# Performance work log

Measured on AMD Instinct MI355X. Metric: run time of the kernel, lower is better.

The kernel has to match this reference:

```python
import jax, jax.numpy as jnp
import numpy as np

G = 4          # conv groups (hardcoded in module)
C = 1024       # channels (hardcoded cin=cout=1024)
SCALE = 1.0 / np.sqrt(1024.0).astype(np.float32)  # 1/sqrt(c/h), h=1


def grouped_proj(x, W, b):
    # pointwise grouped Conv1d == block-diagonal matmul over channel groups
    # x: [B, C, P], W: [G, C//G out, C//G in], b: [C]
    B, C_, P = x.shape
    xg = x.reshape(B, G, C_ // G, P)
    y = jnp.einsum('goi,bgip->bgop', W, xg)  # [B, G, C//G, P]
    return y.reshape(B, C_, P) + b[None, :, None]


def setup_inputs() -> dict:
    key = jax.random.key(0)
    ks = jax.random.split(key, 8)
    B, PK, PQ = 8, 1024, 4096
    cg = C // G
    w_std = 1.0 / np.sqrt(cg).astype(np.float32)  # ~ conv default init scale
    return {
        'Xq': jax.random.normal(ks[0], (B, C, PQ), jnp.float32),
        'Xk': jax.random.normal(ks[1], (B, C, PK), jnp.float32),
        'Wq': jax.random.normal(ks[2], (G, cg, cg), jnp.float32) * w_std,
        'bq': jax.random.normal(ks[3], (C,), jnp.float32) * 0.01,
        'Wk': jax.random.normal(ks[4], (G, cg, cg), jnp.float32) * w_std,
        'bk': jax.random.normal(ks[5], (C,), jnp.float32) * 0.01,
        'Wv': jax.random.normal(ks[6], (G, cg, cg), jnp.float32) * w_std,
        'bv': jax.random.normal(ks[7], (C,), jnp.float32) * 0.01,
    }


def reference(Xq, Xk, Wq, bq, Wk, bk, Wv, bv):
    # Q and K are both projected from Xk; V from Xq (as in the torch code)
    Q = grouped_proj(Xk, Wq, bq)   # [B, C, Pk]
    K = grouped_proj(Xk, Wk, bk)   # [B, C, Pk]
    V = grouped_proj(Xq, Wv, bv)   # [B, C, Pq]
    b, c, pk = K.shape
    pq = V.shape[-1]
    h = 1
    Qh = Q.reshape(b, h, c // h, pk)
    Kh = K.reshape(b, h, c // h, pk)
    Vh = V.reshape(b, h, c // h, pq)
    # H: [B, h, Pk, Pq], contraction over channels; softmax over dim=-2 (Pk)
    H = jnp.einsum('bhci,bhcj->bhij', Kh, Vh) * SCALE
    H = jax.nn.softmax(H, axis=-2)
    # sparse_constrain: Gram over last axis vs identity, mean squared error
    mid = jnp.einsum('bhci,bhki->bhck', H, H)          # [B, h, Pk, Pk]
    Iden = jnp.eye(pk, dtype=H.dtype)[None, None]       # broadcast over B, h
    sparse_loss = jnp.mean((mid - Iden) ** 2)
    # out: mix Q along Pk with attention H -> [B, h, C, Pq]
    out = jnp.einsum('bhij,bhki->bhkj', H, Qh).reshape(b, c, pq)
    return out, sparse_loss, H
```

## Files before the change

### kernel.cpp

```cpp
#include <hip/hip_runtime.h>

typedef _Float16 f16;
typedef f16 f16x4 __attribute__((ext_vector_type(4)));
typedef f16 f16x8 __attribute__((ext_vector_type(8)));
typedef float f32x4 __attribute__((ext_vector_type(4)));

__device__ __forceinline__ void gload16(const void* g, void* ldsbase) {
  __builtin_amdgcn_global_load_lds((const __attribute__((address_space(1))) unsigned int*)g,
                                   (__attribute__((address_space(3))) unsigned int*)ldsbase, 16, 0, 0);
}

__device__ __forceinline__ int swz(int row, int c) {
  return row * 64 + ((c ^ ((row >> 1) & 3)) << 4);
}

template<int MODE>
__global__ void __launch_bounds__(512, 2)
gemm256(const f16* __restrict__ A, const f16* __restrict__ Bm, float* __restrict__ Cf,
        f16* __restrict__ E16, f16* __restrict__ E16t,
        int K, long sA, long sB, float scale, float* __restrict__ aux) {
  __shared__ f16 sb[65536];
  const int t = threadIdx.x, l = t & 63, w = t >> 6;
  const int wr = w >> 2, wc = w & 3;
  const int bid = blockIdx.x;
  const int swzb = (bid & 7) * 64 + (bid >> 3);
  const long b = swzb >> 6;
  const int inner = swzb & 63;
  const int bx = inner >> 2, by = inner & 3;
  const char* Abyte = (const char*)(A + b * sA + (long)(by * 256) * K);
  const char* Bbyte = (const char*)(Bm + b * sB + (long)(bx * 256) * K);

  int offSrc[4];
#pragma unroll
  for (int i = 0; i < 4; ++i) {
    int cid = i * 512 + t, row = cid >> 3, slot = cid & 7;
    offSrc[i] = row * (K * 2) + ((slot ^ (row & 7)) << 4);
  }
  int offAf[8][2], offBf[4][2];
#pragma unroll
  for (int mi = 0; mi < 8; ++mi) {
    int r = wr * 128 + mi * 16 + (l & 15);
#pragma unroll
    for (int ks = 0; ks < 2; ++ks)
      offAf[mi][ks] = r * 64 + ((((ks << 2) + (l >> 4)) ^ (r & 7)) << 3);
  }
#pragma unroll
  for (int ni = 0; ni < 4; ++ni) {
    int r = wc * 64 + ni * 16 + (l & 15);
#pragma unroll
    for (int ks = 0; ks < 2; ++ks)
      offBf[ni][ks] = r * 64 + ((((ks << 2) + (l >> 4)) ^ (r & 7)) << 3);
  }

  const int NT = K >> 6;
  f32x4 acc[8][4] = {};

  auto STAGE = [&](int kt, int bsel) {
    f16* la = sb + bsel * 32768;
    f16* lb = la + 16384;
    const char* as = Abyte + (long)kt * 128;
    const char* bs = Bbyte + (long)kt * 128;
#pragma unroll
    for (int i = 0; i < 4; ++i)
      gload16(as + offSrc[i], la + (i * 512 + (w << 6)) * 8);
#pragma unroll
    for (int i = 0; i < 4; ++i)
      gload16(bs + offSrc[i], lb + (i * 512 + (w << 6)) * 8);
  };

  STAGE(0, 0);
  for (int kt = 0; kt < NT; ++kt) {
    const int cur = kt & 1;
    if (kt + 1 < NT) {
      STAGE(kt + 1, cur ^ 1);
      asm volatile("s_waitcnt vmcnt(8)" ::: "memory");
    } else {
      asm volatile("s_waitcnt vmcnt(0)" ::: "memory");
    }
    __builtin_amdgcn_s_barrier();
    asm volatile("" ::: "memory");
    const f16* la = sb + cur * 32768;
    const f16* lb = la + 16384;
#pragma unroll
    for (int ks = 0; ks < 2; ++ks) {
      f16x8 bf[4];
#pragma unroll
      for (int ni = 0; ni < 4; ++ni) bf[ni] = *(const f16x8*)(lb + offBf[ni][ks]);
#pragma unroll
      for (int mi = 0; mi < 8; ++mi) {
        f16x8 af = *(const f16x8*)(la + offAf[mi][ks]);
#pragma unroll
        for (int ni = 0; ni < 4; ++ni)
          acc[mi][ni] = __builtin_amdgcn_mfma_f32_16x16x32_f16(af, bf[ni], acc[mi][ni], 0, 0, 0);
      }
    }
    asm volatile("s_waitcnt lgkmcnt(0)" ::: "memory");
    __builtin_amdgcn_s_barrier();
    asm volatile("" ::: "memory");
  }

  const int i0 = by * 256, j0 = bx * 256;
  if (MODE == 2) {
    float csum[4] = {};
#pragma unroll
    for (int mi = 0; mi < 8; ++mi)
#pragma unroll
      for (int ni = 0; ni < 4; ++ni)
#pragma unroll
        for (int q = 0; q < 4; ++q) {
          float e = __expf(acc[mi][ni][q] * scale);
          acc[mi][ni][q] = e;
          csum[ni] += e;
        }
#pragma unroll
    for (int ni = 0; ni < 4; ++ni) {
      csum[ni] += __shfl_xor(csum[ni], 16);
      csum[ni] += __shfl_xor(csum[ni], 32);
    }
    float* colp = (float*)(sb + 34816);
    if (l < 16) {
#pragma unroll
      for (int ni = 0; ni < 4; ++ni) colp[wr * 256 + wc * 64 + ni * 16 + l] = csum[ni];
    }
    __syncthreads();
    if (t < 256) aux[(b * 4 + by) * 4096 + bx * 256 + t] = colp[t] + colp[256 + t];
    f16* E16b = E16 + b * 4194304L;
    f16* E16tb = E16t + b * 4194304L;
#pragma unroll
    for (int s = 0; s < 4; ++s) {
      if (wr == (s >> 1)) {
        const int h = s & 1;
#pragma unroll
        for (int m2 = 0; m2 < 4; ++m2)
#pragma unroll
          for (int ni = 0; ni < 4; ++ni)
#pragma unroll
            for (int q = 0; q < 4; ++q)
              sb[(m2 * 16 + (l >> 4) * 4 + q) * 264 + wc * 64 + ni * 16 + (l & 15)] =
                  (f16)acc[h * 4 + m2][ni][q];
      }
      __syncthreads();
#pragma unroll
      for (int ii = 0; ii < 4; ++ii) {
        int cid = ii * 512 + t, r = cid >> 5, cc = cid & 31;
        *(f16x8*)(E16b + (long)(i0 + s * 64 + r) * 4096 + j0 + cc * 8) =
            *(const f16x8*)(sb + r * 264 + cc * 8);
      }
      const int q4 = w >> 1, r8 = l >> 3, ic = l & 7;
#pragma unroll
      for (int ii = 0; ii < 4; ++ii) {
        int j = q4 * 64 + r8 * 8 + (w & 1) * 4 + ii;
        f16x8 v;
#pragma unroll
        for (int k2 = 0; k2 < 8; ++k2) v[k2] = sb[(ic * 8 + k2) * 264 + j];
        *(f16x8*)(E16tb + (long)(j0 + j) * 1024 + i0 + s * 64 + ic * 8) = v;
      }
      __syncthreads();
    }
  } else {
    const float* ip = aux + b * 4096 + bx * 256 + wc * 64;
    float iv[4];
#pragma unroll
    for (int ni = 0; ni < 4; ++ni) iv[ni] = ip[ni * 16 + (l & 15)];
    float* Cb = Cf + b * 4194304L + (long)(by * 256 + wr * 128) * 4096 + bx * 256 + wc * 64;
#pragma unroll
    for (int mi = 0; mi < 8; ++mi)
#pragma unroll
      for (int ni = 0; ni < 4; ++ni)
#pragma unroll
        for (int q = 0; q < 4; ++q)
          Cb[(long)(mi * 16 + (l >> 4) * 4 + q) * 4096 + ni * 16 + (l & 15)] = acc[mi][ni][q] * iv[ni];
  }
}

__global__ void __launch_bounds__(512, 2)
gram_p(const f16* __restrict__ E, const f16* __restrict__ inv2sg,
       float* __restrict__ Hf, float* __restrict__ parts) {
  __shared__ f16 sb[69632];
  const int t = threadIdx.x, l = t & 63, w = t >> 6;
  const int wr = w >> 2, wc = w & 3;
  const int bid = blockIdx.x;
  const long b = bid & 7;
  const int inner = bid >> 3;
  const int by = inner >> 2, bx = inner & 3;
  const char* Abyte = (const char*)(E + b * 4194304L + (long)(by * 256) * 4096);
  const char* Bbyte = (const char*)(E + b * 4194304L + (long)(bx * 256) * 4096);
  f16* invl = sb + 65536;
  gload16((const char*)(inv2sg + b * 4096) + (long)t * 16, invl + (w << 6) * 8);
  int offSrc[4];
#pragma unroll
  for (int i = 0; i < 4; ++i) {
    int cid = i * 512 + t, row = cid >> 3, slot = cid & 7;
    offSrc[i] = row * 8192 + ((slot ^ (row & 7)) << 4);
  }
  int offAf[8][2], offBf[4][2];
#pragma unroll
  for (int mi = 0; mi < 8; ++mi) {
    int r = wr * 128 + mi * 16 + (l & 15);
#pragma unroll
    for (int ks = 0; ks < 2; ++ks)
      offAf[mi][ks] = r * 64 + ((((ks << 2) + (l >> 4)) ^ (r & 7)) << 3);
  }
#pragma unroll
  for (int ni = 0; ni < 4; ++ni) {
    int r = wc * 64 + ni * 16 + (l & 15);
#pragma unroll
    for (int ks = 0; ks < 2; ++ks)
      offBf[ni][ks] = r * 64 + ((((ks << 2) + (l >> 4)) ^ (r & 7)) << 3);
  }
  f32x4 acc[8][4] = {};
  auto STAGE = [&](int kt, int bsel) {
    f16* la = sb + bsel * 32768;
    f16* lb = la + 16384;
    const char* as = Abyte + (long)kt * 128;
    const char* bs = Bbyte + (long)kt * 128;
#pragma unroll
    for (int i = 0; i < 4; ++i) gload16(as + offSrc[i], la + (i * 512 + (w << 6)) * 8);
#pragma unroll
    for (int i = 0; i < 4; ++i) gload16(bs + offSrc[i], lb + (i * 512 + (w << 6)) * 8);
  };
  const int kw0 = bx * 16;
  STAGE(0, 0);
  for (int kt = 0; kt < 64; ++kt) {
    const int cur = kt & 1;
    if (kt + 1 < 64) {
      STAGE(kt + 1, cur ^ 1);
      if (kt - 1 >= kw0 && kt - 1 < kw0 + 16) asm volatile("s_waitcnt vmcnt(40)" ::: "memory");
      else                                    asm volatile("s_waitcnt vmcnt(8)" ::: "memory");
    } else {
      asm volatile("s_waitcnt vmcnt(0)" ::: "memory");
    }
    __builtin_amdgcn_s_barrier();
    asm volatile("" ::: "memory");
    const f16* la = sb + cur * 32768;
    const f16* lb = la + 16384;
#pragma unroll
    for (int ks = 0; ks < 2; ++ks) {
      const f16x8 invv = *(const f16x8*)(invl + kt * 64 + ks * 32 + ((l >> 4) << 3));
      f16x8 bf[4];
#pragma unroll
      for (int ni = 0; ni < 4; ++ni) bf[ni] = *(const f16x8*)(lb + offBf[ni][ks]);
#pragma unroll
      for (int mi = 0; mi < 8; ++mi) {
        f16x8 af = *(const f16x8*)(la + offAf[mi][ks]) * invv;
#pragma unroll
        for (int ni = 0; ni < 4; ++ni)
          acc[mi][ni] = __builtin_amdgcn_mfma_f32_16x16x32_f16(af, bf[ni], acc[mi][ni], 0, 0, 0);
      }
    }
    if (kt >= kw0 && kt < kw0 + 16) {
      const float iv = sqrtf((float)invl[kt * 64 + l]) * (1.0f / 64.0f);
      float* hp = Hf + b * 4194304L + (long)(by * 256 + w * 32) * 4096 + kt * 64 + l;
#pragma unroll
      for (int rr = 0; rr < 32; ++rr) {
        const int row = w * 32 + rr;
        f16 ev = la[row * 64 + ((((l >> 3) ^ (row & 7)) << 3) | (l & 7))];
        hp[(long)rr * 4096] = (float)ev * iv;
      }
    }
    asm volatile("s_waitcnt lgkmcnt(0)" ::: "memory");
    __builtin_amdgcn_s_barrier();
    asm volatile("" ::: "memory");
  }
  const int gr0 = by * 256 + wr * 128 + (l >> 4) * 4;
  const int gc0 = bx * 256 + wc * 64 + (l & 15);
  float p = 0.f;
#pragma unroll
  for (int mi = 0; mi < 8; ++mi)
#pragma unroll
    for (int ni = 0; ni < 4; ++ni)
#pragma unroll
      for (int q = 0; q < 4; ++q) {
        float e = acc[mi][ni][q] * (1.0f / 4096.0f);
        if (gr0 + mi * 16 + q == gc0 + ni * 16) e -= 1.f;
        p += e * e;
      }
#pragma unroll
  for (int d = 32; d; d >>= 1) p += __shfl_down(p, d);
  __shared__ float red[8];
  if (l == 0) red[w] = p;
  __syncthreads();
  if (t == 0) {
    float s = 0.f;
#pragma unroll
    for (int i = 0; i < 8; ++i) s += red[i];
    parts[bid] = s;
  }
}

__global__ void __launch_bounds__(512)
proj_qk(const float* __restrict__ X, const f16* __restrict__ Wq16, const f16* __restrict__ Wk16,
        const float* __restrict__ bq, const float* __restrict__ bk,
        f16* __restrict__ Q, f16* __restrict__ Kt) {
  __shared__ f16 sb[20480];
  f16* Wqs = sb;
  f16* Wks = sb + 8192;
  f16* Xs = sb + 16384;
  const int t = threadIdx.x, l = t & 63, w = t >> 6;
  const int wrq = w >> 1, wcq = w & 1;
  const int bg = blockIdx.z, g = bg & 3;
  const long b = bg >> 2;
  const int p0 = blockIdx.x * 128;
  const float* Xb = X + b * 1048576 + (long)g * 262144;
  const char* WqB = (const char*)(Wq16 + g * 65536);
  const char* WkB = (const char*)(Wk16 + g * 65536);
  int wOff[2];
#pragma unroll
  for (int i = 0; i < 2; ++i) {
    int c = i * 512 + t, row = c >> 2, slot = (c & 3) ^ ((row >> 1) & 3);
    wOff[i] = row * 512 + (slot << 4);
  }
  const int xp = t & 127, xc = t >> 7;
  const float* xS = Xb + (long)(xc * 8) * 1024 + p0 + xp;
  const int xo = swz(xp, xc);
  int offW[4], offX[4];
#pragma unroll
  for (int i = 0; i < 4; ++i) {
    int rc = wrq * 64 + i * 16 + (l & 15);
    offW[i] = swz(rc, l >> 4);
    int rp = wcq * 64 + i * 16 + (l & 15);
    offX[i] = swz(rp, l >> 4);
  }
  f32x4 accq[4][4] = {}, acck[4][4] = {};
  for (int k0 = 0; k0 < 256; k0 += 32) {
#pragma unroll
    for (int i = 0; i < 2; ++i) {
      gload16(WqB + wOff[i] + k0 * 2, Wqs + (i * 512 + (w << 6)) * 8);
      gload16(WkB + wOff[i] + k0 * 2, Wks + (i * 512 + (w << 6)) * 8);
    }
    const float* xs = xS + (long)k0 * 1024;
    f16x8 v;
#pragma unroll
    for (int d = 0; d < 8; ++d) v[d] = (f16)xs[(long)d * 1024];
    *(f16x8*)((char*)Xs + xo) = v;
    __syncthreads();
    f16x8 qf[4], kf[4], xf[4];
#pragma unroll
    for (int i = 0; i < 4; ++i) {
      qf[i] = *(const f16x8*)((const char*)Wqs + offW[i]);
      kf[i] = *(const f16x8*)((const char*)Wks + offW[i]);
      xf[i] = *(const f16x8*)((const char*)Xs + offX[i]);
    }
#pragma unroll
    for (int mi = 0; mi < 4; ++mi)
#pragma unroll
      for (int ni = 0; ni < 4; ++ni) {
        accq[mi][ni] = __builtin_amdgcn_mfma_f32_16x16x32_f16(qf[mi], xf[ni], accq[mi][ni], 0, 0, 0);
        acck[ni][mi] = __builtin_amdgcn_mfma_f32_16x16x32_f16(xf[ni], kf[mi], acck[ni][mi], 0, 0, 0);
      }
    __syncthreads();
  }
  f16* Qb = Q + b * 1048576 + (long)(g * 256 + wrq * 64) * 1024 + p0 + wcq * 64;
#pragma unroll
  for (int mi = 0; mi < 4; ++mi)
#pragma unroll
    for (int q = 0; q < 4; ++q) {
      float bv = bq[g * 256 + wrq * 64 + mi * 16 + (l >> 4) * 4 + q];
#pragma unroll
      for (int ni = 0; ni < 4; ++ni)
        Qb[(long)(mi * 16 + (l >> 4) * 4 + q) * 1024 + ni * 16 + (l & 15)] = (f16)(accq[mi][ni][q] + bv);
    }
  f16* Kb = Kt + b * 1048576 + (long)(p0 + wcq * 64) * 1024 + g * 256 + wrq * 64;
  float bcol[4];
#pragma unroll
  for (int ni = 0; ni < 4; ++ni) bcol[ni] = bk[g * 256 + wrq * 64 + ni * 16 + (l & 15)];
#pragma unroll
  for (int mi = 0; mi < 4; ++mi)
#pragma unroll
    for (int q = 0; q < 4; ++q)
#pragma unroll
      for (int ni = 0; ni < 4; ++ni)
        Kb[(long)(mi * 16 + (l >> 4) * 4 + q) * 1024 + ni * 16 + (l & 15)] = (f16)(acck[mi][ni][q] + bcol[ni]);
}

__global__ void __launch_bounds__(512)
proj_v(const float* __restrict__ X, const f16* __restrict__ Wv16, const float* __restrict__ bv,
       f16* __restrict__ Vt) {
  __shared__ f16 sb[12288];
  f16* Wvs = sb;
  f16* Xs = sb + 8192;
  const int t = threadIdx.x, l = t & 63, w = t >> 6;
  const int wrq = w >> 1, wcq = w & 1;
  const int bg = blockIdx.z, g = bg & 3;
  const long b = bg >> 2;
  const int p0 = blockIdx.x * 128;
  const float* Xb = X + b * 4194304 + (long)g * 1048576;
  const char* WvB = (const char*)(Wv16 + g * 65536);
  int wOff[2];
#pragma unroll
  for (int i = 0; i < 2; ++i) {
    int c = i * 512 + t, row = c >> 2, slot = (c & 3) ^ ((row >> 1) & 3);
    wOff[i] = row * 512 + (slot << 4);
  }
  const int xp = t & 127, xc = t >> 7;
  const float* xS = Xb + (long)(xc * 8) * 4096 + p0 + xp;
  const int xo = swz(xp, xc);
  int offW[4], offX[4];
#pragma unroll
  for (int i = 0; i < 4; ++i) {
    int rc = wrq * 64 + i * 16 + (l & 15);
    offW[i] = swz(rc, l >> 4);
    int rp = wcq * 64 + i * 16 + (l & 15);
    offX[i] = swz(rp, l >> 4);
  }
  f32x4 acc[4][4] = {};
  for (int k0 = 0; k0 < 256; k0 += 32) {
#pragma unroll
    for (int i = 0; i < 2; ++i)
      gload16(WvB + wOff[i] + k0 * 2, Wvs + (i * 512 + (w << 6)) * 8);
    const float* xs = xS + (long)k0 * 4096;
    f16x8 v;
#pragma unroll
    for (int d = 0; d < 8; ++d) v[d] = (f16)xs[(long)d * 4096];
    *(f16x8*)((char*)Xs + xo) = v;
    __syncthreads();
    f16x8 wf[4], xf[4];
#pragma unroll
    for (int i = 0; i < 4; ++i) {
      wf[i] = *(const f16x8*)((const char*)Wvs + offW[i]);
      xf[i] = *(const f16x8*)((const char*)Xs + offX[i]);
    }
#pragma unroll
    for (int mi = 0; mi < 4; ++mi)
#pragma unroll
      for (int ni = 0; ni < 4; ++ni)
        acc[mi][ni] = __builtin_amdgcn_mfma_f32_16x16x32_f16(xf[mi], wf[ni], acc[mi][ni], 0, 0, 0);
    __syncthreads();
  }
  f16* Vb = Vt + b * 4194304 + (long)(p0 + wcq * 64) * 1024 + g * 256 + wrq * 64;
  float bcol[4];
#pragma unroll
  for (int ni = 0; ni < 4; ++ni) bcol[ni] = bv[g * 256 + wrq * 64 + ni * 16 + (l & 15)];
#pragma unroll
  for (int mi = 0; mi < 4; ++mi)
#pragma unroll
    for (int q = 0; q < 4; ++q)
#pragma unroll
      for (int ni = 0; ni < 4; ++ni)
        Vb[(long)(mi * 16 + (l >> 4) * 4 + q) * 1024 + ni * 16 + (l & 15)] = (f16)(acc[mi][ni][q] + bcol[ni]);
}

__global__ void __launch_bounds__(256)
inv_k(const float* __restrict__ colsum, float* __restrict__ inv, f16* __restrict__ inv2s) {
  int gid = blockIdx.x * 256 + threadIdx.x;
  int b = gid >> 12, j = gid & 4095;
  const float* cp = colsum + (long)(b * 4) * 4096 + j;
  float s = 0.f;
#pragma unroll
  for (int my = 0; my < 4; ++my) s += cp[my * 4096];
  float iv = 1.f / s;
  inv[gid] = iv;
  inv2s[gid] = (f16)(iv * iv * 4096.0f);
}

__global__ void cvt3(const float* __restrict__ a, const float* __restrict__ b2,
                     const float* __restrict__ c, f16* __restrict__ da,
                     f16* __restrict__ db, f16* __restrict__ dc) {
  int i = blockIdx.x * 256 + threadIdx.x;
  int which = i >> 18, r = i & 262143;
  if (which == 0) da[r] = (f16)a[r];
  else if (which == 1) db[r] = (f16)b2[r];
  else dc[r] = (f16)c[r];
}

__global__ void __launch_bounds__(256)
finalize_k(const float* __restrict__ parts, float* __restrict__ o) {
  const int t = threadIdx.x;
  float s = (t < 128) ? parts[t] : 0.f;
#pragma unroll
  for (int d = 32; d; d >>= 1) s += __shfl_down(s, d);
  __shared__ float red[4];
  if ((t & 63) == 0) red[t >> 6] = s;
  __syncthreads();
  if (t == 0) *o = (red[0] + red[1] + red[2] + red[3]) * (1.0f / 8388608.0f);
}

extern "C" void kernel_launch(void* const* d_in, const int* in_sizes, int n_in,
                              void* d_out, int out_size, void* d_ws, size_t ws_size,
                              hipStream_t stream) {
  const float* Xq = (const float*)d_in[0];
  const float* Xk = (const float*)d_in[1];
  const float* Wq = (const float*)d_in[2];
  const float* bq = (const float*)d_in[3];
  const float* Wk = (const float*)d_in[4];
  const float* bk = (const float*)d_in[5];
  const float* Wv = (const float*)d_in[6];
  const float* bv = (const float*)d_in[7];
  float* out = (float*)d_out;
  float* loss_out = out + 33554432;
  float* Hf = out + 33554433;

  char* ws = (char*)d_ws;
  f16* W16q = (f16*)(ws);
  f16* W16k = (f16*)(ws + (1 << 19));
  f16* W16v = (f16*)(ws + 2L * (1 << 19));
  f16* Q16  = (f16*)(ws + 3L * (1 << 19));
  f16* Kt16 = (f16*)(ws + 3L * (1 << 19) + (1L << 24));
  f16* Vt16 = (f16*)(ws + 3L * (1 << 19) + 2L * (1 << 24));
  f16* E16  = (f16*)(ws + 3L * (1 << 19) + 2L * (1 << 24) + (1L << 26));
  f16* E16t = (f16*)(ws + 3L * (1 << 19) + 2L * (1 << 24) + 2L * (1 << 26));
  char* tail = ws + 3L * (1 << 19) + 2L * (1 << 24) + 3L * (1 << 26);
  float* parts = (float*)tail;
  float* invb  = (float*)(tail + 8192);
  f16*   inv2s = (f16*)(tail + 8192 + 131072);
  float* colsum = (float*)(ws);

  cvt3<<<3072, 256, 0, stream>>>(Wq, Wk, Wv, W16q, W16k, W16v);

  proj_qk<<<dim3(8, 1, 32), 512, 0, stream>>>(Xk, W16q, W16k, bq, bk, Q16, Kt16);
  proj_v <<<dim3(32, 1, 32), 512, 0, stream>>>(Xq, W16v, bv, Vt16);

  gemm256<2><<<512, 512, 0, stream>>>(Kt16, Vt16, nullptr, E16, E16t,
      1024, 1L << 20, 1L << 22, 0.03125f, colsum);

  inv_k<<<128, 256, 0, stream>>>(colsum, invb, inv2s);

  gemm256<3><<<512, 512, 0, stream>>>(Q16, E16t, out, nullptr, nullptr,
      1024, 1L << 20, 1L << 22, 1.0f, invb);

  gram_p<<<128, 512, 0, stream>>>(E16, inv2s, Hf, parts);
  finalize_k<<<1, 256, 0, stream>>>(parts, loss_out);
}
```

Measured before the change: 436.2 us.

## Merge output GEMM and Gram-loss kernels into one launch with heterogeneous blocks

```diff
diff --git a/kernel.cpp b/kernel.cpp
--- a/kernel.cpp
+++ b/kernel.cpp
@@ -157,134 +157,208 @@
       }
       __syncthreads();
     }
-  } else {
-    const float* ip = aux + b * 4096 + bx * 256 + wc * 64;
-    float iv[4];
-#pragma unroll
-    for (int ni = 0; ni < 4; ++ni) iv[ni] = ip[ni * 16 + (l & 15)];
-    float* Cb = Cf + b * 4194304L + (long)(by * 256 + wr * 128) * 4096 + bx * 256 + wc * 64;
-#pragma unroll
-    for (int mi = 0; mi < 8; ++mi)
-#pragma unroll
-      for (int ni = 0; ni < 4; ++ni)
-#pragma unroll
-        for (int q = 0; q < 4; ++q)
-          Cb[(long)(mi * 16 + (l >> 4) * 4 + q) * 4096 + ni * 16 + (l & 15)] = acc[mi][ni][q] * iv[ni];
   }
 }
 
 __global__ void __launch_bounds__(512, 2)
-gram_p(const f16* __restrict__ E, const f16* __restrict__ inv2sg,
+fused3(const f16* __restrict__ Q, const f16* __restrict__ Et, float* __restrict__ Cf,
+       const float* __restrict__ invg,
+       const f16* __restrict__ E, const f16* __restrict__ inv2sg,
        float* __restrict__ Hf, float* __restrict__ parts) {
   __shared__ f16 sb[69632];
   const int t = threadIdx.x, l = t & 63, w = t >> 6;
   const int wr = w >> 2, wc = w & 3;
-  const int bid = blockIdx.x;
-  const long b = bid & 7;
-  const int inner = bid >> 3;
-  const int by = inner >> 2, bx = inner & 3;
-  const char* Abyte = (const char*)(E + b * 4194304L + (long)(by * 256) * 4096);
-  const char* Bbyte = (const char*)(E + b * 4194304L + (long)(bx * 256) * 4096);
-  f16* invl = sb + 65536;
-  gload16((const char*)(inv2sg + b * 4096) + (long)t * 16, invl + (w << 6) * 8);
-  int offSrc[4];
-#pragma unroll
-  for (int i = 0; i < 4; ++i) {
-    int cid = i * 512 + t, row = cid >> 3, slot = cid & 7;
-    offSrc[i] = row * 8192 + ((slot ^ (row & 7)) << 4);
-  }
-  int offAf[8][2], offBf[4][2];
-#pragma unroll
-  for (int mi = 0; mi < 8; ++mi) {
-    int r = wr * 128 + mi * 16 + (l & 15);
-#pragma unroll
-    for (int ks = 0; ks < 2; ++ks)
-      offAf[mi][ks] = r * 64 + ((((ks << 2) + (l >> 4)) ^ (r & 7)) << 3);
-  }
-#pragma unroll
-  for (int ni = 0; ni < 4; ++ni) {
-    int r = wc * 64 + ni * 16 + (l & 15);
-#pragma unroll
-    for (int ks = 0; ks < 2; ++ks)
-      offBf[ni][ks] = r * 64 + ((((ks << 2) + (l >> 4)) ^ (r & 7)) << 3);
-  }
-  f32x4 acc[8][4] = {};
-  auto STAGE = [&](int kt, int bsel) {
-    f16* la = sb + bsel * 32768;
-    f16* lb = la + 16384;
-    const char* as = Abyte + (long)kt * 128;
-    const char* bs = Bbyte + (long)kt * 128;
-#pragma unroll
-    for (int i = 0; i < 4; ++i) gload16(as + offSrc[i], la + (i * 512 + (w << 6)) * 8);
-#pragma unroll
-    for (int i = 0; i < 4; ++i) gload16(bs + offSrc[i], lb + (i * 512 + (w << 6)) * 8);
-  };
-  const int kw0 = bx * 16;
-  STAGE(0, 0);
-  for (int kt = 0; kt < 64; ++kt) {
-    const int cur = kt & 1;
-    if (kt + 1 < 64) {
-      STAGE(kt + 1, cur ^ 1);
-      if (kt - 1 >= kw0 && kt - 1 < kw0 + 16) asm volatile("s_waitcnt vmcnt(40)" ::: "memory");
-      else                                    asm volatile("s_waitcnt vmcnt(8)" ::: "memory");
-    } else {
-      asm volatile("s_waitcnt vmcnt(0)" ::: "memory");
-    }
-    __builtin_amdgcn_s_barrier();
-    asm volatile("" ::: "memory");
-    const f16* la = sb + cur * 32768;
-    const f16* lb = la + 16384;
-#pragma unroll
-    for (int ks = 0; ks < 2; ++ks) {
-      const f16x8 invv = *(const f16x8*)(invl + kt * 64 + ks * 32 + ((l >> 4) << 3));
-      f16x8 bf[4];
-#pragma unroll
-      for (int ni = 0; ni < 4; ++ni) bf[ni] = *(const f16x8*)(lb + offBf[ni][ks]);
-#pragma unroll
-      for (int mi = 0; mi < 8; ++mi) {
-        f16x8 af = *(const f16x8*)(la + offAf[mi][ks]) * invv;
-#pragma unroll
-        for (int ni = 0; ni < 4; ++ni)
-          acc[mi][ni] = __builtin_amdgcn_mfma_f32_16x16x32_f16(af, bf[ni], acc[mi][ni], 0, 0, 0);
-      }
-    }
-    if (kt >= kw0 && kt < kw0 + 16) {
-      const float iv = sqrtf((float)invl[kt * 64 + l]) * (1.0f / 64.0f);
-      float* hp = Hf + b * 4194304L + (long)(by * 256 + w * 32) * 4096 + kt * 64 + l;
-#pragma unroll
-      for (int rr = 0; rr < 32; ++rr) {
-        const int row = w * 32 + rr;
-        f16 ev = la[row * 64 + ((((l >> 3) ^ (row & 7)) << 3) | (l & 7))];
-        hp[(long)rr * 4096] = (float)ev * iv;
-      }
-    }
-    asm volatile("s_waitcnt lgkmcnt(0)" ::: "memory");
-    __builtin_amdgcn_s_barrier();
-    asm volatile("" ::: "memory");
-  }
-  const int gr0 = by * 256 + wr * 128 + (l >> 4) * 4;
-  const int gc0 = bx * 256 + wc * 64 + (l & 15);
-  float p = 0.f;
-#pragma unroll
-  for (int mi = 0; mi < 8; ++mi)
-#pragma unroll
-    for (int ni = 0; ni < 4; ++ni)
-#pragma unroll
-      for (int q = 0; q < 4; ++q) {
-        float e = acc[mi][ni][q] * (1.0f / 4096.0f);
-        if (gr0 + mi * 16 + q == gc0 + ni * 16) e -= 1.f;
-        p += e * e;
-      }
-#pragma unroll
-  for (int d = 32; d; d >>= 1) p += __shfl_down(p, d);
-  __shared__ float red[8];
-  if (l == 0) red[w] = p;
-  __syncthreads();
-  if (t == 0) {
-    float s = 0.f;
-#pragma unroll
-    for (int i = 0; i < 8; ++i) s += red[i];
-    parts[bid] = s;
+
+  if (blockIdx.x < 128) {
+    const int bid = blockIdx.x;
+    const long b = bid & 7;
+    const int inner = bid >> 3;
+    const int by = inner >> 2, bx = inner & 3;
+    const char* Abyte = (const char*)(E + b * 4194304L + (long)(by * 256) * 4096);
+    const char* Bbyte = (const char*)(E + b * 4194304L + (long)(bx * 256) * 4096);
+    f16* invl = sb + 65536;
+    gload16((const char*)(inv2sg + b * 4096) + (long)t * 16, invl + (w << 6) * 8);
+    int offSrc[4];
+#pragma unroll
+    for (int i = 0; i < 4; ++i) {
+      int cid = i * 512 + t, row = cid >> 3, slot = cid & 7;
+      offSrc[i] = row * 8192 + ((slot ^ (row & 7)) << 4);
+    }
+    int offAf[8][2], offBf[4][2];
+#pragma unroll
+    for (int mi = 0; mi < 8; ++mi) {
+      int r = wr * 128 + mi * 16 + (l & 15);
+#pragma unroll
+      for (int ks = 0; ks < 2; ++ks)
+        offAf[mi][ks] = r * 64 + ((((ks << 2) + (l >> 4)) ^ (r & 7)) << 3);
+    }
+#pragma unroll
+    for (int ni = 0; ni < 4; ++ni) {
+      int r = wc * 64 + ni * 16 + (l & 15);
+#pragma unroll
+      for (int ks = 0; ks < 2; ++ks)
+        offBf[ni][ks] = r * 64 + ((((ks << 2) + (l >> 4)) ^ (r & 7)) << 3);
+    }
+    f32x4 acc[8][4] = {};
+    auto STAGE = [&](int kt, int bsel) {
+      f16* la = sb + bsel * 32768;
+      f16* lb = la + 16384;
+      const char* as = Abyte + (long)kt * 128;
+      const char* bs = Bbyte + (long)kt * 128;
+#pragma unroll
+      for (int i = 0; i < 4; ++i) gload16(as + offSrc[i], la + (i * 512 + (w << 6)) * 8);
+#pragma unroll
+      for (int i = 0; i < 4; ++i) gload16(bs + offSrc[i], lb + (i * 512 + (w << 6)) * 8);
+    };
+    const int kw0 = bx * 16;
+    STAGE(0, 0);
+    for (int kt = 0; kt < 64; ++kt) {
+      const int cur = kt & 1;
+      if (kt + 1 < 64) {
+        STAGE(kt + 1, cur ^ 1);
+        if (kt - 1 >= kw0 && kt - 1 < kw0 + 16) asm volatile("s_waitcnt vmcnt(40)" ::: "memory");
+        else                                    asm volatile("s_waitcnt vmcnt(8)" ::: "memory");
+      } else {
+        asm volatile("s_waitcnt vmcnt(0)" ::: "memory");
+      }
+      __builtin_amdgcn_s_barrier();
+      asm volatile("" ::: "memory");
+      const f16* la = sb + cur * 32768;
+      const f16* lb = la + 16384;
+#pragma unroll
+      for (int ks = 0; ks < 2; ++ks) {
+        const f16x8 invv = *(const f16x8*)(invl + kt * 64 + ks * 32 + ((l >> 4) << 3));
+        f16x8 bf[4];
+#pragma unroll
+        for (int ni = 0; ni < 4; ++ni) bf[ni] = *(const f16x8*)(lb + offBf[ni][ks]);
+#pragma unroll
+        for (int mi = 0; mi < 8; ++mi) {
+          f16x8 af = *(const f16x8*)(la + offAf[mi][ks]) * invv;
+#pragma unroll
+          for (int ni = 0; ni < 4; ++ni)
+            acc[mi][ni] = __builtin_amdgcn_mfma_f32_16x16x32_f16(af, bf[ni], acc[mi][ni], 0, 0, 0);
+        }
+      }
+      if (kt >= kw0 && kt < kw0 + 16) {
+        const float iv = sqrtf((float)invl[kt * 64 + l]) * (1.0f / 64.0f);
+        float* hp = Hf + b * 4194304L + (long)(by * 256 + w * 32) * 4096 + kt * 64 + l;
+#pragma unroll
+        for (int rr = 0; rr < 32; ++rr) {
+          const int row = w * 32 + rr;
+          f16 ev = la[row * 64 + ((((l >> 3) ^ (row & 7)) << 3) | (l & 7))];
+          hp[(long)rr * 4096] = (float)ev * iv;
+        }
+      }
+      asm volatile("s_waitcnt lgkmcnt(0)" ::: "memory");
+      __builtin_amdgcn_s_barrier();
+      asm volatile("" ::: "memory");
+    }
+    const int gr0 = by * 256 + wr * 128 + (l >> 4) * 4;
+    const int gc0 = bx * 256 + wc * 64 + (l & 15);
+    float p = 0.f;
+#pragma unroll
+    for (int mi = 0; mi < 8; ++mi)
+#pragma unroll
+      for (int ni = 0; ni < 4; ++ni)
+#pragma unroll
+        for (int q = 0; q < 4; ++q) {
+          float e = acc[mi][ni][q] * (1.0f / 4096.0f);
+          if (gr0 + mi * 16 + q == gc0 + ni * 16) e -= 1.f;
+          p += e * e;
+        }
+#pragma unroll
+    for (int d = 32; d; d >>= 1) p += __shfl_down(p, d);
+    __shared__ float red[8];
+    if (l == 0) red[w] = p;
+    __syncthreads();
+    if (t == 0) {
+      float s = 0.f;
+#pragma unroll
+      for (int i = 0; i < 8; ++i) s += red[i];
+      parts[bid] = s;
+    }
+  } else {
+    const int bid = blockIdx.x - 128;
+    const int swzb = (bid & 7) * 64 + (bid >> 3);
+    const long b = swzb >> 6;
+    const int inner = swzb & 63;
+    const int bx = inner >> 2, by = inner & 3;
+    const char* Abyte = (const char*)(Q + b * 1048576L + (long)(by * 256) * 1024);
+    const char* Bbyte = (const char*)(Et + b * 4194304L + (long)(bx * 256) * 1024);
+    int offSrc[4];
+#pragma unroll
+    for (int i = 0; i < 4; ++i) {
+      int cid = i * 512 + t, row = cid >> 3, slot = cid & 7;
+      offSrc[i] = row * 2048 + ((slot ^ (row & 7)) << 4);
+    }
+    int offAf[8][2], offBf[4][2];
+#pragma unroll
+    for (int mi = 0; mi < 8; ++mi) {
+      int r = wr * 128 + mi * 16 + (l & 15);
+#pragma unroll
+      for (int ks = 0; ks < 2; ++ks)
+        offAf[mi][ks] = r * 64 + ((((ks << 2) + (l >> 4)) ^ (r & 7)) << 3);
+    }
+#pragma unroll
+    for (int ni = 0; ni < 4; ++ni) {
+      int r = wc * 64 + ni * 16 + (l & 15);
+#pragma unroll
+      for (int ks = 0; ks < 2; ++ks)
+        offBf[ni][ks] = r * 64 + ((((ks << 2) + (l >> 4)) ^ (r & 7)) << 3);
+    }
+    f32x4 acc[8][4] = {};
+    auto STAGE = [&](int kt, int bsel) {
+      f16* la = sb + bsel * 32768;
+      f16* lb = la + 16384;
+      const char* as = Abyte + (long)kt * 128;
+      const char* bs = Bbyte + (long)kt * 128;
+#pragma unroll
+      for (int i = 0; i < 4; ++i) gload16(as + offSrc[i], la + (i * 512 + (w << 6)) * 8);
+#pragma unroll
+      for (int i = 0; i < 4; ++i) gload16(bs + offSrc[i], lb + (i * 512 + (w << 6)) * 8);
+    };
+    STAGE(0, 0);
+    for (int kt = 0; kt < 16; ++kt) {
+      const int cur = kt & 1;
+      if (kt + 1 < 16) {
+        STAGE(kt + 1, cur ^ 1);
+        asm volatile("s_waitcnt vmcnt(8)" ::: "memory");
+      } else {
+        asm volatile("s_waitcnt vmcnt(0)" ::: "memory");
+      }
+      __builtin_amdgcn_s_barrier();
+      asm volatile("" ::: "memory");
+      const f16* la = sb + cur * 32768;
+      const f16* lb = la + 16384;
+#pragma unroll
+      for (int ks = 0; ks < 2; ++ks) {
+        f16x8 bf[4];
+#pragma unroll
+        for (int ni = 0; ni < 4; ++ni) bf[ni] = *(const f16x8*)(lb + offBf[ni][ks]);
+#pragma unroll
+        for (int mi = 0; mi < 8; ++mi) {
+          f16x8 af = *(const f16x8*)(la + offAf[mi][ks]);
+#pragma unroll
+          for (int ni = 0; ni < 4; ++ni)
+            acc[mi][ni] = __builtin_amdgcn_mfma_f32_16x16x32_f16(af, bf[ni], acc[mi][ni], 0, 0, 0);
+        }
+      }
+      asm volatile("s_waitcnt lgkmcnt(0)" ::: "memory");
+      __builtin_amdgcn_s_barrier();
+      asm volatile("" ::: "memory");
+    }
+    const float* ip = invg + b * 4096 + bx * 256 + wc * 64;
+    float iv[4];
+#pragma unroll
+    for (int ni = 0; ni < 4; ++ni) iv[ni] = ip[ni * 16 + (l & 15)];
+    float* Cb = Cf + b * 4194304L + (long)(by * 256 + wr * 128) * 4096 + bx * 256 + wc * 64;
+#pragma unroll
+    for (int mi = 0; mi < 8; ++mi)
+#pragma unroll
+      for (int ni = 0; ni < 4; ++ni)
+#pragma unroll
+        for (int q = 0; q < 4; ++q)
+          Cb[(long)(mi * 16 + (l >> 4) * 4 + q) * 4096 + ni * 16 + (l & 15)] = acc[mi][ni][q] * iv[ni];
   }
 }
 
@@ -515,9 +589,6 @@
 
   inv_k<<<128, 256, 0, stream>>>(colsum, invb, inv2s);
 
-  gemm256<3><<<512, 512, 0, stream>>>(Q16, E16t, out, nullptr, nullptr,
-      1024, 1L << 20, 1L << 22, 1.0f, invb);
-
-  gram_p<<<128, 512, 0, stream>>>(E16, inv2s, Hf, parts);
+  fused3<<<640, 512, 0, stream>>>(Q16, E16t, out, invb, E16, inv2s, Hf, parts);
   finalize_k<<<1, 256, 0, stream>>>(parts, loss_out);
 }
```

Result: faster. 375.2 us (-14.0%).
